# Performance work log

Measured on AMD Instinct MI355X. Metric: run time of the kernel, lower is better.

## Reference

```python
import math
import jax, jax.numpy as jnp
import numpy as np

H = 16  # num_attention_heads
D = 64  # attention_head_size
ALPHA = 32.0  # PB-relax alpha


def setup_inputs() -> dict:
    key = jax.random.key(0)
    ks = jax.random.split(key, 8)
    B, S, C = 4, 1024, 1024
    scale = 1.0 / math.sqrt(C)
    return {
        "hidden_states": jax.random.normal(ks[0], (B, S, C), jnp.float32),
        "attention_mask": jnp.zeros((B, 1, 1, S), jnp.float32),
        "rel_pos": jax.random.normal(ks[1], (B, H, S, S), jnp.float32),
        "rel_2d_pos": jax.random.normal(ks[2], (B, H, S, S), jnp.float32),
        "Wq": jax.random.normal(ks[3], (C, C), jnp.float32) * scale,
        "bq": jnp.zeros((C,), jnp.float32),
        "Wk": jax.random.normal(ks[4], (C, C), jnp.float32) * scale,
        "bk": jnp.zeros((C,), jnp.float32),
        "Wv": jax.random.normal(ks[5], (C, C), jnp.float32) * scale,
        "bv": jnp.zeros((C,), jnp.float32),
    }


def _heads(x, B, S):
    # [B,S,C] -> [B,H,S,D]
    return x.reshape(B, S, H, D).transpose(0, 2, 1, 3)


def cogview_softmax(scores):
    # PB-relax: softmax(((s/alpha) - max(s/alpha)) * alpha)
    s = scores / ALPHA
    m = jnp.max(s, axis=-1, keepdims=True)
    return jax.nn.softmax((s - m) * ALPHA, axis=-1)


def reference(hidden_states, attention_mask, rel_pos, rel_2d_pos,
              Wq, bq, Wk, bk, Wv, bv):
    B, S, C = hidden_states.shape
    inv_sqrt_d = 1.0 / math.sqrt(D)
    # torch nn.Linear: y = x @ W.T + b; here W is stored as [out, in]
    q = _heads(hidden_states @ Wq.T + bq, B, S)  # [B,H,S,D]
    k = _heads(hidden_states @ Wk.T + bk, B, S)
    v = _heads(hidden_states @ Wv.T + bv, B, S)

    scores = jnp.einsum('bhqd,bhkd->bhqk', q * inv_sqrt_d, k)
    scores = scores + (rel_pos + rel_2d_pos) * inv_sqrt_d
    scores = scores + attention_mask  # broadcast [B,1,1,S]

    probs = cogview_softmax(scores)  # dropout prob = 0 (eval)
    ctx = jnp.einsum('bhqk,bhkd->bhqd', probs, v)
    ctx = ctx.transpose(0, 2, 1, 3).reshape(B, S, C)
    return ctx
```

## Files before the change

kernel.cpp:

```cpp
#include <hip/hip_runtime.h>
#include <hip/hip_bf16.h>

typedef __attribute__((ext_vector_type(8))) short bf16x8;
typedef __attribute__((ext_vector_type(4))) float f32x4;

#define LDSG(g, l) __builtin_amdgcn_global_load_lds(                      \
    (const __attribute__((address_space(1))) void*)(g),                   \
    (__attribute__((address_space(3))) void*)(l), 16, 0, 0)

#define LOG2E 1.44269504088896f
#define RELSC 0.180336880111112f

__global__ __launch_bounds__(256) void cvt_kernel(
    const float* __restrict__ hs,
    const float* __restrict__ wq, const float* __restrict__ wk,
    const float* __restrict__ wv,
    __hip_bfloat16* __restrict__ hbf, __hip_bfloat16* __restrict__ wbf)
{
  const int NH = (4 * 1024 * 1024) / 4;
  const int NW = (1024 * 1024) / 4;
  int i = blockIdx.x * 256 + threadIdx.x;
  float4 v;
  __hip_bfloat16* dst;
  if (i < NH) {
    v = ((const float4*)hs)[i];
    dst = hbf + (size_t)i * 4;
  } else {
    int j = i - NH;
    int which = j / NW, r = j - which * NW;
    const float* src = which == 0 ? wq : (which == 1 ? wk : wv);
    v = ((const float4*)src)[r];
    dst = wbf + (size_t)j * 4;
  }
  union { ushort4 u; __hip_bfloat16 b[4]; } o;
  o.b[0] = __float2bfloat16(v.x);
  o.b[1] = __float2bfloat16(v.y);
  o.b[2] = __float2bfloat16(v.z);
  o.b[3] = __float2bfloat16(v.w);
  *((ushort4*)dst) = o.u;
}

__global__ __launch_bounds__(256) void qkv_gemm(
    const __hip_bfloat16* __restrict__ A,
    const __hip_bfloat16* __restrict__ W,
    const float* __restrict__ bq, const float* __restrict__ bk,
    const float* __restrict__ bv,
    __hip_bfloat16* __restrict__ qo, __hip_bfloat16* __restrict__ ko,
    __hip_bfloat16* __restrict__ vo)
{
  const int K = 1024;
  __shared__ __hip_bfloat16 As[128 * 64];
  __shared__ __hip_bfloat16 Bs[128 * 64];
  const int bid = blockIdx.x;
  const int bm = bid & 31, bn = bid >> 5;
  const int m0 = bm * 128, n0 = bn * 128;
  const int tid = threadIdx.x, wid = tid >> 6, lane = tid & 63;
  const int wm = wid >> 1, wn = wid & 1;

  f32x4 acc[4][4] = {};

  const int srow = lane >> 3;
  const int schunk = (lane & 7) ^ srow;

  for (int k0 = 0; k0 < K; k0 += 64) {
#pragma unroll
    for (int p = 0; p < 4; ++p) {
      int r = (wid * 4 + p) * 8 + srow;
      LDSG(&A[(size_t)(m0 + r) * K + k0 + schunk * 8], &As[(wid * 4 + p) * 512]);
      LDSG(&W[(size_t)(n0 + r) * K + k0 + schunk * 8], &Bs[(wid * 4 + p) * 512]);
    }
    __syncthreads();
#pragma unroll
    for (int ks = 0; ks < 2; ++ks) {
      bf16x8 af[4], bfr[4];
#pragma unroll
      for (int mi = 0; mi < 4; ++mi) {
        int row = wm * 64 + mi * 16 + (lane & 15);
        int slot = (ks * 4 + (lane >> 4)) ^ (lane & 7);
        af[mi] = *(const bf16x8*)((const char*)As + row * 128 + slot * 16);
      }
#pragma unroll
      for (int ni = 0; ni < 4; ++ni) {
        int row = wn * 64 + ni * 16 + (lane & 15);
        int slot = (ks * 4 + (lane >> 4)) ^ (lane & 7);
        bfr[ni] = *(const bf16x8*)((const char*)Bs + row * 128 + slot * 16);
      }
#pragma unroll
      for (int mi = 0; mi < 4; ++mi)
#pragma unroll
        for (int ni = 0; ni < 4; ++ni)
          acc[mi][ni] = __builtin_amdgcn_mfma_f32_16x16x32_bf16(
              af[mi], bfr[ni], acc[mi][ni], 0, 0, 0);
    }
    __syncthreads();
  }

#pragma unroll
  for (int ni = 0; ni < 4; ++ni) {
    int n = n0 + wn * 64 + ni * 16 + (lane & 15);
    int which = n >> 10;
    int h = (n >> 6) & 15;
    int d = n & 63;
    const float* bias = which == 0 ? bq : (which == 1 ? bk : bv);
    float bval = bias[n & 1023];
    if (which == 0) {
#pragma unroll
      for (int mi = 0; mi < 4; ++mi) {
#pragma unroll
        for (int j = 0; j < 4; ++j) {
          int m = m0 + wm * 64 + mi * 16 + (lane >> 4) * 4 + j;
          int b = m >> 10, s = m & 1023;
          float val = (acc[mi][ni][j] + bval) * RELSC;
          qo[(((size_t)(b * 16 + h) << 10) + s) * 64 + d] = __float2bfloat16(val);
        }
      }
    } else if (which == 1) {
      int dks = d >> 5, dlg = (d >> 3) & 3, de = d & 7;
#pragma unroll
      for (int mi = 0; mi < 4; ++mi) {
#pragma unroll
        for (int j = 0; j < 4; ++j) {
          int m = m0 + wm * 64 + mi * 16 + (lane >> 4) * 4 + j;
          int b = m >> 10, s = m & 1023;
          size_t idx = ((((size_t)(b * 16 + h)) * 16 + (s >> 6)) * 512 +
                        (size_t)((dks * 4 + ((s >> 4) & 3)) * 64 + (s & 15) +
                                 16 * dlg)) * 8 + de;
          ko[idx] = __float2bfloat16(acc[mi][ni][j] + bval);
        }
      }
    } else {
      int dt = d >> 4, dl15 = d & 15;
#pragma unroll
      for (int mi = 0; mi < 4; ++mi) {
        int m = m0 + wm * 64 + mi * 16 + (lane >> 4) * 4;
        int b = m >> 10, k = m & 1023;
        int kt = k >> 6, kks = (k >> 5) & 1, klg = (k >> 3) & 3, ke = k & 7;
        union { ushort4 u; __hip_bfloat16 bb[4]; } o;
#pragma unroll
        for (int j = 0; j < 4; ++j)
          o.bb[j] = __float2bfloat16(acc[mi][ni][j] + bval);
        size_t idx = ((((size_t)(b * 16 + h)) * 16 + kt) * 512 +
                      (size_t)((kks * 4 + dt) * 64 + dl15 + 16 * klg)) * 8 + ke;
        *(ushort4*)&vo[idx] = o.u;
      }
    }
  }
}

__global__ __launch_bounds__(256, 2) void attn_kernel(
    const __hip_bfloat16* __restrict__ qg, const __hip_bfloat16* __restrict__ kf,
    const __hip_bfloat16* __restrict__ vf,
    const float* __restrict__ rel1, const float* __restrict__ rel2,
    const float* __restrict__ mask, float* __restrict__ out)
{
  __shared__ float Rbuf[2][4][2][16][64];
  __shared__ float Ml[1024];
  __shared__ __hip_bfloat16 Ps[2][16 * 64];

  const int bid = blockIdx.x;
  const int bh = bid & 63, qt = bid >> 6;
  const int b = bh >> 4, h = bh & 15;
  const int tid = threadIdx.x, wid = tid >> 6, lane = tid & 63;
  const int lg = lane >> 4, ln15 = lane & 15;

  const size_t qbase = (size_t)bh << 16;
  const size_t fbase = (size_t)bh << 16;

  if (wid >= 2) {
    const int cw = wid - 2;
    const int q0c = qt * 32 + cw * 16;
    const int r4 = lane >> 4, c15 = lane & 15;
    const float* relw1 = rel1 + ((size_t)bh << 20);
    const float* relw2 = rel2 + ((size_t)bh << 20);

    {
      int i = cw * 64 + lane;
      float4 m0 = *(const float4*)&mask[((size_t)b << 10) + i * 8];
      float4 m1 = *(const float4*)&mask[((size_t)b << 10) + i * 8 + 4];
      float4 s0, s1;
      s0.x = m0.x * LOG2E - 32.0f; s0.y = m0.y * LOG2E - 32.0f;
      s0.z = m0.z * LOG2E - 32.0f; s0.w = m0.w * LOG2E - 32.0f;
      s1.x = m1.x * LOG2E - 32.0f; s1.y = m1.y * LOG2E - 32.0f;
      s1.z = m1.z * LOG2E - 32.0f; s1.w = m1.w * LOG2E - 32.0f;
      *(float4*)&Ml[i * 8] = s0;
      *(float4*)&Ml[i * 8 + 4] = s1;
    }

#define SREL(T) do {                                                        \
    _Pragma("unroll") for (int p = 0; p < 4; ++p) {                         \
      int rg = 4 * p + r4;                                                  \
      int cg = c15 ^ (rg & 7);                                              \
      LDSG(&relw1[(size_t)(q0c + rg) * 1024 + (T) * 64 + cg * 4],           \
           &Rbuf[cw][(T) & 3][0][4 * p][0]);                                \
      LDSG(&relw2[(size_t)(q0c + rg) * 1024 + (T) * 64 + cg * 4],           \
           &Rbuf[cw][(T) & 3][1][4 * p][0]);                                \
    } } while (0)

    SREL(0); SREL(1); SREL(2);
    __builtin_amdgcn_sched_barrier(0);
    asm volatile("s_waitcnt vmcnt(16) lgkmcnt(0)" ::: "memory");
    __builtin_amdgcn_s_barrier();

#pragma unroll
    for (int t = 0; t <= 12; ++t) {
      SREL(t + 3);
      __builtin_amdgcn_sched_barrier(0);
      asm volatile("s_waitcnt vmcnt(16)" ::: "memory");
      __builtin_amdgcn_s_barrier();
    }
    asm volatile("s_waitcnt vmcnt(8)" ::: "memory");
    __builtin_amdgcn_s_barrier();
    asm volatile("s_waitcnt vmcnt(0)" ::: "memory");
    __builtin_amdgcn_s_barrier();
    return;
  }

  const int q0 = qt * 32 + wid * 16;

  bf16x8 qf[2];
  qf[0] = *(const bf16x8*)&qg[qbase + (size_t)(q0 + ln15) * 64 + lg * 8];
  qf[1] = *(const bf16x8*)&qg[qbase + (size_t)(q0 + ln15) * 64 + 32 + lg * 8];

  bf16x8 kA[8], vA[8], kB[8], vB[8];
#pragma unroll
  for (int i = 0; i < 8; ++i)
    kA[i] = *(const bf16x8*)&kf[fbase + i * 512 + lane * 8];
#pragma unroll
  for (int i = 0; i < 8; ++i)
    vA[i] = *(const bf16x8*)&vf[fbase + i * 512 + lane * 8];

  f32x4 accO[4] = {};
  float lrun = 0.f;

  __builtin_amdgcn_s_barrier();

#define CBODY(KC, VC, KN, VN, T, PF) do {                                   \
    f32x4 st[4] = {};                                                       \
    _Pragma("unroll") for (int ks = 0; ks < 2; ++ks)                        \
      _Pragma("unroll") for (int ct = 0; ct < 4; ++ct)                      \
        st[ct] = __builtin_amdgcn_mfma_f32_16x16x32_bf16(                   \
            KC[ks * 4 + ct], qf[ks], st[ct], 0, 0, 0);                      \
    if (PF) {                                                               \
      _Pragma("unroll") for (int i = 0; i < 8; ++i)                         \
        KN[i] = *(const bf16x8*)&kf[fbase + (size_t)((T) + 1) * 4096 +      \
                                    i * 512 + lane * 8];                    \
      _Pragma("unroll") for (int i = 0; i < 8; ++i)                         \
        VN[i] = *(const bf16x8*)&vf[fbase + (size_t)((T) + 1) * 4096 +      \
                                    i * 512 + lane * 8];                    \
      __builtin_amdgcn_sched_barrier(0);                                    \
    }                                                                       \
    const char* Rb1 = (const char*)&Rbuf[wid][(T) & 3][0][0][0];            \
    const char* Rb2 = (const char*)&Rbuf[wid][(T) & 3][1][0][0];            \
    float p_[4][4];                                                         \
    _Pragma("unroll") for (int ct = 0; ct < 4; ++ct) {                      \
      int cc = ((ct * 4 + lg) ^ (ln15 & 7)) * 16;                           \
      float4 rv1 = *(const float4*)(Rb1 + ln15 * 256 + cc);                 \
      float4 rv2 = *(const float4*)(Rb2 + ln15 * 256 + cc);                 \
      float4 mv = *(const float4*)&Ml[(T) * 64 + ct * 16 + lg * 4];         \
      _Pragma("unroll") for (int j = 0; j < 4; ++j) {                       \
        float sv = st[ct][j] +                                              \
                   RELSC * (((const float*)&rv1)[j] +                       \
                            ((const float*)&rv2)[j]) +                      \
                   ((const float*)&mv)[j];                                  \
        float e = __builtin_amdgcn_exp2f(sv);                               \
        p_[ct][j] = e; lrun += e;                                           \
      }                                                                     \
    }                                                                       \
    __hip_bfloat16* Pw = &Ps[wid][0];                                       \
    _Pragma("unroll") for (int ct = 0; ct < 4; ++ct) {                      \
      union { ushort4 u; __hip_bfloat16 bb[4]; } w;                         \
      _Pragma("unroll") for (int j = 0; j < 4; ++j)                         \
        w.bb[j] = __float2bfloat16(p_[ct][j]);                              \
      *(ushort4*)((char*)Pw + ln15 * 128 +                                  \
                  ((ct * 32 + lg * 8) ^ ((ln15 & 7) << 4))) = w.u;          \
    }                                                                       \
    bf16x8 pt[2];                                                           \
    pt[0] = *(const bf16x8*)((const char*)Pw + ln15 * 128 +                 \
                             ((lg * 16) ^ ((ln15 & 7) << 4)));              \
    pt[1] = *(const bf16x8*)((const char*)Pw + ln15 * 128 +                 \
                             ((64 + lg * 16) ^ ((ln15 & 7) << 4)));         \
    _Pragma("unroll") for (int ks = 0; ks < 2; ++ks)                        \
      _Pragma("unroll") for (int dt = 0; dt < 4; ++dt)                      \
        accO[dt] = __builtin_amdgcn_mfma_f32_16x16x32_bf16(                 \
            VC[ks * 4 + dt], pt[ks], accO[dt], 0, 0, 0);                    \
    if ((T) < 15) __builtin_amdgcn_s_barrier();                             \
  } while (0)

  for (int t = 0; t < 7; ++t) {
    CBODY(kA, vA, kB, vB, 2 * t, 1);
    CBODY(kB, vB, kA, vA, 2 * t + 1, 1);
  }
  CBODY(kA, vA, kB, vB, 14, 1);
  CBODY(kB, vB, kA, vA, 15, 0);

  lrun += __shfl_xor(lrun, 16, 64);
  lrun += __shfl_xor(lrun, 32, 64);
  float rl = 1.0f / lrun;

#pragma unroll
  for (int dt = 0; dt < 4; ++dt) {
    float4 o;
    o.x = accO[dt][0] * rl;
    o.y = accO[dt][1] * rl;
    o.z = accO[dt][2] * rl;
    o.w = accO[dt][3] * rl;
    *(float4*)&out[((size_t)(b * 1024 + q0 + ln15)) * 1024 + h * 64 +
                   dt * 16 + lg * 4] = o;
  }
}

extern "C" void kernel_launch(void* const* d_in, const int* in_sizes, int n_in,
                              void* d_out, int out_size, void* d_ws,
                              size_t ws_size, hipStream_t stream) {
  const float* hs   = (const float*)d_in[0];
  const float* mask = (const float*)d_in[1];
  const float* rel1 = (const float*)d_in[2];
  const float* rel2 = (const float*)d_in[3];
  const float* Wq   = (const float*)d_in[4];
  const float* bq   = (const float*)d_in[5];
  const float* Wk   = (const float*)d_in[6];
  const float* bk   = (const float*)d_in[7];
  const float* Wv   = (const float*)d_in[8];
  const float* bv   = (const float*)d_in[9];

  char* ws = (char*)d_ws;
  __hip_bfloat16* hbf = (__hip_bfloat16*)(ws);
  __hip_bfloat16* wbf = (__hip_bfloat16*)(ws + 8388608);
  __hip_bfloat16* qb  = (__hip_bfloat16*)(ws + 14680064);
  __hip_bfloat16* kfb = (__hip_bfloat16*)(ws + 23068672);
  __hip_bfloat16* vfb = (__hip_bfloat16*)(ws + 31457280);

  cvt_kernel<<<7168, 256, 0, stream>>>(hs, Wq, Wk, Wv, hbf, wbf);
  qkv_gemm<<<768, 256, 0, stream>>>(hbf, wbf, bq, bk, bv, qb, kfb, vfb);
  attn_kernel<<<2048, 256, 0, stream>>>(qb, kfb, vfb, rel1, rel2, mask,
                                        (float*)d_out);
}
```

Before: 182.1 us.

## Split attention key range across four compute waves with 8-query tiles

The attention kernel now uses 384-thread blocks, each covering 8 query rows. Four compute waves each handle a disjoint quarter of the key tiles, and two loader waves stage the full 8x1024 rel_pos rows into LDS in two halves. Partial outputs and row sums are reduced through LDS at the end, replacing the sequential per-wave sweep over all 16 key tiles. This raises parallelism and drops the K/V double-buffer pipeline. The cost is half-wasted MFMA rows (only 8 of 16 used), four times more blocks re-reading K/V, and an added cross-wave reduction.

```diff
diff --git a/kernel.cpp b/kernel.cpp
--- a/kernel.cpp
+++ b/kernel.cpp
@@ -147,15 +147,16 @@
   }
 }
 
-__global__ __launch_bounds__(256, 2) void attn_kernel(
+__global__ __launch_bounds__(384, 3) void attn_kernel(
     const __hip_bfloat16* __restrict__ qg, const __hip_bfloat16* __restrict__ kf,
     const __hip_bfloat16* __restrict__ vf,
     const float* __restrict__ rel1, const float* __restrict__ rel2,
     const float* __restrict__ mask, float* __restrict__ out)
 {
-  __shared__ float Rbuf[2][4][2][16][64];
+  __shared__ float Rp[2][8][1024];
   __shared__ float Ml[1024];
-  __shared__ __hip_bfloat16 Ps[2][16 * 64];
+  __shared__ __hip_bfloat16 Ps[4][16 * 64];
+  __shared__ float Lr[4][16];
 
   const int bid = blockIdx.x;
   const int bh = bid & 63, qt = bid >> 6;
@@ -165,16 +166,15 @@
 
   const size_t qbase = (size_t)bh << 16;
   const size_t fbase = (size_t)bh << 16;
-
-  if (wid >= 2) {
-    const int cw = wid - 2;
-    const int q0c = qt * 32 + cw * 16;
-    const int r4 = lane >> 4, c15 = lane & 15;
-    const float* relw1 = rel1 + ((size_t)bh << 20);
-    const float* relw2 = rel2 + ((size_t)bh << 20);
+  const int q0 = qt * 8;
+
+  if (wid >= 4) {
+    const int s = wid - 4;
+    const float* relw0 = rel1 + ((size_t)bh << 20);
+    const float* relw1 = rel2 + ((size_t)bh << 20);
 
     {
-      int i = cw * 64 + lane;
+      int i = s * 64 + lane;
       float4 m0 = *(const float4*)&mask[((size_t)b << 10) + i * 8];
       float4 m1 = *(const float4*)&mask[((size_t)b << 10) + i * 8 + 4];
       float4 s0, s1;
@@ -186,76 +186,56 @@
       *(float4*)&Ml[i * 8 + 4] = s1;
     }
 
-#define SREL(T) do {                                                        \
-    _Pragma("unroll") for (int p = 0; p < 4; ++p) {                         \
-      int rg = 4 * p + r4;                                                  \
-      int cg = c15 ^ (rg & 7);                                              \
-      LDSG(&relw1[(size_t)(q0c + rg) * 1024 + (T) * 64 + cg * 4],           \
-           &Rbuf[cw][(T) & 3][0][4 * p][0]);                                \
-      LDSG(&relw2[(size_t)(q0c + rg) * 1024 + (T) * 64 + cg * 4],           \
-           &Rbuf[cw][(T) & 3][1][4 * p][0]);                                \
+#define SHALF(H) do {                                                       \
+    _Pragma("unroll") for (int rr = 0; rr < 4; ++rr) {                      \
+      int r = s * 4 + rr;                                                   \
+      int soff = ((lane & 56) | ((lane ^ r) & 7)) * 4;                      \
+      _Pragma("unroll") for (int P = 0; P < 2; ++P) {                       \
+        LDSG(&relw0[(size_t)(q0 + r) * 1024 + (H) * 512 + P * 256 + soff],  \
+             &Rp[0][r][(H) * 512 + P * 256]);                               \
+        LDSG(&relw1[(size_t)(q0 + r) * 1024 + (H) * 512 + P * 256 + soff],  \
+             &Rp[1][r][(H) * 512 + P * 256]);                               \
+      }                                                                     \
     } } while (0)
 
-    SREL(0); SREL(1); SREL(2);
-    __builtin_amdgcn_sched_barrier(0);
-    asm volatile("s_waitcnt vmcnt(16) lgkmcnt(0)" ::: "memory");
+    SHALF(0);
+    asm volatile("s_waitcnt vmcnt(0) lgkmcnt(0)" ::: "memory");
     __builtin_amdgcn_s_barrier();
-
-#pragma unroll
-    for (int t = 0; t <= 12; ++t) {
-      SREL(t + 3);
-      __builtin_amdgcn_sched_barrier(0);
-      asm volatile("s_waitcnt vmcnt(16)" ::: "memory");
-      __builtin_amdgcn_s_barrier();
-    }
-    asm volatile("s_waitcnt vmcnt(8)" ::: "memory");
-    __builtin_amdgcn_s_barrier();
+    SHALF(1);
     asm volatile("s_waitcnt vmcnt(0)" ::: "memory");
     __builtin_amdgcn_s_barrier();
+    __builtin_amdgcn_s_barrier();
     return;
   }
 
-  const int q0 = qt * 32 + wid * 16;
-
+  const int qrow = q0 + (ln15 & 7);
   bf16x8 qf[2];
-  qf[0] = *(const bf16x8*)&qg[qbase + (size_t)(q0 + ln15) * 64 + lg * 8];
-  qf[1] = *(const bf16x8*)&qg[qbase + (size_t)(q0 + ln15) * 64 + 32 + lg * 8];
-
-  bf16x8 kA[8], vA[8], kB[8], vB[8];
-#pragma unroll
-  for (int i = 0; i < 8; ++i)
-    kA[i] = *(const bf16x8*)&kf[fbase + i * 512 + lane * 8];
-#pragma unroll
-  for (int i = 0; i < 8; ++i)
-    vA[i] = *(const bf16x8*)&vf[fbase + i * 512 + lane * 8];
+  qf[0] = *(const bf16x8*)&qg[qbase + (size_t)qrow * 64 + lg * 8];
+  qf[1] = *(const bf16x8*)&qg[qbase + (size_t)qrow * 64 + 32 + lg * 8];
 
   f32x4 accO[4] = {};
   float lrun = 0.f;
-
-  __builtin_amdgcn_s_barrier();
-
-#define CBODY(KC, VC, KN, VN, T, PF) do {                                   \
+  const int r_ = ln15 & 7;
+
+#define CB(T) do {                                                          \
+    bf16x8 kfr[8], vfr[8];                                                  \
+    _Pragma("unroll") for (int i = 0; i < 8; ++i)                           \
+      kfr[i] = *(const bf16x8*)&kf[fbase + (size_t)(T) * 4096 + i * 512 +   \
+                                   lane * 8];                               \
+    _Pragma("unroll") for (int i = 0; i < 8; ++i)                           \
+      vfr[i] = *(const bf16x8*)&vf[fbase + (size_t)(T) * 4096 + i * 512 +   \
+                                   lane * 8];                               \
     f32x4 st[4] = {};                                                       \
     _Pragma("unroll") for (int ks = 0; ks < 2; ++ks)                        \
       _Pragma("unroll") for (int ct = 0; ct < 4; ++ct)                      \
         st[ct] = __builtin_amdgcn_mfma_f32_16x16x32_bf16(                   \
-            KC[ks * 4 + ct], qf[ks], st[ct], 0, 0, 0);                      \
-    if (PF) {                                                               \
-      _Pragma("unroll") for (int i = 0; i < 8; ++i)                         \
-        KN[i] = *(const bf16x8*)&kf[fbase + (size_t)((T) + 1) * 4096 +      \
-                                    i * 512 + lane * 8];                    \
-      _Pragma("unroll") for (int i = 0; i < 8; ++i)                         \
-        VN[i] = *(const bf16x8*)&vf[fbase + (size_t)((T) + 1) * 4096 +      \
-                                    i * 512 + lane * 8];                    \
-      __builtin_amdgcn_sched_barrier(0);                                    \
-    }                                                                       \
-    const char* Rb1 = (const char*)&Rbuf[wid][(T) & 3][0][0][0];            \
-    const char* Rb2 = (const char*)&Rbuf[wid][(T) & 3][1][0][0];            \
+            kfr[ks * 4 + ct], qf[ks], st[ct], 0, 0, 0);                     \
     float p_[4][4];                                                         \
     _Pragma("unroll") for (int ct = 0; ct < 4; ++ct) {                      \
-      int cc = ((ct * 4 + lg) ^ (ln15 & 7)) * 16;                           \
-      float4 rv1 = *(const float4*)(Rb1 + ln15 * 256 + cc);                 \
-      float4 rv2 = *(const float4*)(Rb2 + ln15 * 256 + cc);                 \
+      int cc = (T) * 16 + ct * 4 + lg;                                      \
+      int phys = (cc & ~7) | ((cc ^ r_) & 7);                               \
+      float4 rv1 = *(const float4*)((const char*)&Rp[0][r_][0] + phys * 16);\
+      float4 rv2 = *(const float4*)((const char*)&Rp[1][r_][0] + phys * 16);\
       float4 mv = *(const float4*)&Ml[(T) * 64 + ct * 16 + lg * 4];         \
       _Pragma("unroll") for (int j = 0; j < 4; ++j) {                       \
         float sv = st[ct][j] +                                              \
@@ -282,30 +262,45 @@
     _Pragma("unroll") for (int ks = 0; ks < 2; ++ks)                        \
       _Pragma("unroll") for (int dt = 0; dt < 4; ++dt)                      \
         accO[dt] = __builtin_amdgcn_mfma_f32_16x16x32_bf16(                 \
-            VC[ks * 4 + dt], pt[ks], accO[dt], 0, 0, 0);                    \
-    if ((T) < 15) __builtin_amdgcn_s_barrier();                             \
+            vfr[ks * 4 + dt], pt[ks], accO[dt], 0, 0, 0);                   \
   } while (0)
 
-  for (int t = 0; t < 7; ++t) {
-    CBODY(kA, vA, kB, vB, 2 * t, 1);
-    CBODY(kB, vB, kA, vA, 2 * t + 1, 1);
-  }
-  CBODY(kA, vA, kB, vB, 14, 1);
-  CBODY(kB, vB, kA, vA, 15, 0);
+  __builtin_amdgcn_s_barrier();
+  CB(wid);
+  CB(wid + 4);
+  __builtin_amdgcn_s_barrier();
+  CB(wid + 8);
+  CB(wid + 12);
 
   lrun += __shfl_xor(lrun, 16, 64);
   lrun += __shfl_xor(lrun, 32, 64);
-  float rl = 1.0f / lrun;
-
-#pragma unroll
-  for (int dt = 0; dt < 4; ++dt) {
-    float4 o;
-    o.x = accO[dt][0] * rl;
-    o.y = accO[dt][1] * rl;
-    o.z = accO[dt][2] * rl;
-    o.w = accO[dt][3] * rl;
-    *(float4*)&out[((size_t)(b * 1024 + q0 + ln15)) * 1024 + h * 64 +
-                   dt * 16 + lg * 4] = o;
+  if (lane < 16) Lr[wid][lane] = lrun;
+
+  {
+    float* Od = (float*)&Ps[wid][0];
+    if (ln15 < 8) {
+#pragma unroll
+      for (int dt = 0; dt < 4; ++dt)
+        *(f32x4*)&Od[ln15 * 64 + dt * 16 + lg * 4] = accO[dt];
+    }
+  }
+  asm volatile("s_waitcnt lgkmcnt(0)" ::: "memory");
+  __builtin_amdgcn_s_barrier();
+
+  {
+    int q = 2 * wid + (lane >> 5);
+    int d = (lane & 31) * 2;
+    float ax = 0.f, ay = 0.f, lr = 0.f;
+#pragma unroll
+    for (int w = 0; w < 4; ++w) {
+      const float* Ow = (const float*)&Ps[w][0];
+      float2 v = *(const float2*)&Ow[q * 64 + d];
+      ax += v.x; ay += v.y;
+      lr += Lr[w][q];
+    }
+    float rl = 1.0f / lr;
+    float2 o; o.x = ax * rl; o.y = ay * rl;
+    *(float2*)&out[((size_t)(b * 1024 + q0 + q)) * 1024 + h * 64 + d] = o;
   }
 }
 
@@ -332,6 +327,6 @@
 
   cvt_kernel<<<7168, 256, 0, stream>>>(hs, Wq, Wk, Wv, hbf, wbf);
   qkv_gemm<<<768, 256, 0, stream>>>(hbf, wbf, bq, bk, bv, qb, kfb, vfb);
-  attn_kernel<<<2048, 256, 0, stream>>>(qb, kfb, vfb, rel1, rel2, mask,
+  attn_kernel<<<8192, 384, 0, stream>>>(qb, kfb, vfb, rel1, rel2, mask,
                                         (float*)d_out);
 }
```

Result: slower. 303.3 us (+66.6%).
